# Kernel tuning notes

Measured on AMD Instinct MI355X. Metric: run time of the kernel, lower is better.

## Reference

```python
import jax, jax.numpy as jnp
import numpy as np

# HBV parameter bounds, in the order of self.parameters_bound
BOUNDS = np.array([
    [1.0, 6.0],     # parBETA
    [50.0, 1000.0], # parFC
    [0.05, 0.9],    # parK0
    [0.01, 0.5],    # parK1
    [0.001, 0.2],   # parK2
    [0.2, 1.0],     # parLP
    [0.0, 10.0],    # parPERC
    [0.0, 100.0],   # parUZL
    [-2.5, 2.5],    # parTT
    [0.5, 10.0],    # parCFMAX
    [0.0, 0.1],     # parCFR
    [0.0, 0.2],     # parCWH
    [0.3, 5.0],     # parBETAET
    [0.0, 1.0],     # parC (capillary)
    [0.0, 20.0],    # parTRbound (unused in core recurrence)
    [0.0, 2500.0],  # parAc (unused in core recurrence)
], dtype=np.float32)
NEARZERO = 1e-5
LENF = 15  # unit-hydrograph length
ROUT_A_MAX = 2.9
ROUT_B_MAX = 6.5


def uh_gamma(a, b, lenF):
    # a, b: [Ngrid]; returns normalized gamma UH weights [lenF, Ngrid]
    aa = jax.nn.relu(a) + 0.1
    theta = jax.nn.relu(b) + 0.5
    tt = jnp.arange(0.5, float(lenF), dtype=jnp.float32)[:, None]  # [lenF,1]
    w = jnp.exp(-jax.scipy.special.gammaln(aa)) / (theta ** aa) * tt ** (aa - 1.0) * jnp.exp(-tt / theta)
    return w / w.sum(0)


def hbv_forward(x_hydro_model, params_raw, conv_params_hydro):
    # x_hydro_model: [T, N, 3] (P, Temp, PET); params_raw: [T, N, 16, M]; conv: [N, 2]
    T, N, _ = x_hydro_model.shape
    M = params_raw.shape[-1]
    b = jnp.asarray(BOUNDS)
    p = b[:, 0].reshape(1, 1, -1, 1) + params_raw * (b[:, 1] - b[:, 0]).reshape(1, 1, -1, 1)
    (BETA, FC, K0, K1, K2, LP, PERC, UZL, TT, CFMAX, CFR, CWH, BETAET, C) = [p[:, :, i, :] for i in range(14)]
    Pm = x_hydro_model[:, :, 0:1]    # [T,N,1] broadcast vs nmul
    Tm = x_hydro_model[:, :, 1:2]
    PETm = x_hydro_model[:, :, 2:3]

    init = tuple(jnp.full((N, M), 0.001, jnp.float32) for _ in range(5))

    def step(carry, inp):
        SNOWPACK, MELTWATER, SM, SUZ, SLZ = carry
        (P_, Ta, PET_, BETA_, FC_, K0_, K1_, K2_, LP_, PERC_, UZL_, TT_, CFMAX_, CFR_, CWH_, BETAET_, C_) = inp
        RAIN = jnp.where(Ta >= TT_, P_, 0.0)
        SNOW = jnp.where(Ta < TT_, P_, 0.0)
        # snow routine
        SNOWPACK = SNOWPACK + SNOW
        melt = jnp.minimum(jnp.maximum(CFMAX_ * (Ta - TT_), 0.0), SNOWPACK)
        MELTWATER = MELTWATER + melt
        SNOWPACK = jnp.maximum(SNOWPACK - melt, NEARZERO)
        refreeze = jnp.minimum(jnp.maximum(CFR_ * CFMAX_ * (TT_ - Ta), 0.0), MELTWATER)
        SNOWPACK = SNOWPACK + refreeze
        MELTWATER = jnp.maximum(MELTWATER - refreeze, NEARZERO)
        tosoil = jnp.maximum(MELTWATER - CWH_ * SNOWPACK, 0.0)
        MELTWATER = jnp.maximum(MELTWATER - tosoil, NEARZERO)
        # soil routine
        soil_wet = jnp.clip((SM / FC_) ** BETA_, 0.0, 1.0)
        recharge = (RAIN + tosoil) * soil_wet
        SM = SM + RAIN + tosoil - recharge
        excess = jnp.maximum(SM - FC_, 0.0)
        SM = jnp.maximum(SM - excess, NEARZERO)
        evapfactor = jnp.clip((SM / (LP_ * FC_)) ** BETAET_, 0.0, 1.0)
        ETact = jnp.minimum(SM, PET_ * evapfactor)
        SM = jnp.maximum(SM - ETact, NEARZERO)
        # capillary rise from lower zone (parC)
        capillary = jnp.minimum(SLZ, C_ * SLZ * (1.0 - jnp.minimum(SM / FC_, 1.0)))
        SM = SM + capillary
        SLZ = jnp.maximum(SLZ - capillary, NEARZERO)
        # response routine
        SUZ = SUZ + recharge + excess
        PERCa = jnp.minimum(SUZ, PERC_)
        SUZ = SUZ - PERCa
        Q0 = K0_ * jnp.maximum(SUZ - UZL_, 0.0)
        SUZ = SUZ - Q0
        Q1 = K1_ * SUZ
        SUZ = SUZ - Q1
        SLZ = SLZ + PERCa
        Q2 = K2_ * SLZ
        SLZ = SLZ - Q2
        Qt = (Q0 + Q1 + Q2).mean(-1)  # average over nmul components -> [N]
        return (SNOWPACK, MELTWATER, SM, SUZ, SLZ), Qt

    _, Qsim = jax.lax.scan(step, init, (Pm, Tm, PETm, BETA, FC, K0, K1, K2, LP, PERC, UZL, TT, CFMAX, CFR, CWH, BETAET, C))
    # gamma-UH routing (causal per-grid convolution)
    rout_a = conv_params_hydro[:, 0] * ROUT_A_MAX
    rout_b = conv_params_hydro[:, 1] * ROUT_B_MAX
    UH = uh_gamma(rout_a, rout_b, LENF)  # [LENF, N]
    Qpad = jnp.pad(Qsim, ((LENF - 1, 0), (0, 0)))  # [T+LENF-1, N]
    Qrout = jnp.zeros_like(Qsim)
    for k in range(LENF):  # small fixed kernel length
        Qrout = Qrout + UH[k][None, :] * Qpad[LENF - 1 - k: LENF - 1 - k + T]
    return Qrout  # [T, N]


def setup_inputs() -> dict:
    key = jax.random.key(0)
    k1, k2, k3, k4, k5 = jax.random.split(key, 5)
    T, N, NP, M = 365, 4000, 16, 4
    P = jax.random.uniform(k1, (T, N), jnp.float32) * 15.0        # precip mm/day
    Temp = jax.random.uniform(k2, (T, N), jnp.float32) * 35.0 - 10.0  # deg C
    PET = jax.random.uniform(k3, (T, N), jnp.float32) * 6.0       # mm/day
    x_hydro_model = jnp.stack([P, Temp, PET], axis=-1)             # [T,N,3]
    params_raw = jax.random.uniform(k4, (T, N, NP, M), jnp.float32)
    conv_params_hydro = jax.random.uniform(k5, (N, 2), jnp.float32)
    return {"x_hydro_model": x_hydro_model, "params_raw": params_raw, "conv_params_hydro": conv_params_hydro}


def reference(x_hydro_model, params_raw, conv_params_hydro):
    return hbv_forward(x_hydro_model, params_raw, conv_params_hydro)
```

## Files before the change

### kernel.cpp

```cpp
#include <hip/hip_runtime.h>
#include <math.h>

#define NEARZERO 1e-5f
#define LENF 15

#define KB 7
#define CHUNK_STRIDE (1024 + 16)
#define SLOT_PARAM (4 * CHUNK_STRIDE)
#define SLOT_BYTES (SLOT_PARAM + 192)
#define BUF_BYTES (KB * SLOT_BYTES)
#define LDS_BYTES (2 * BUF_BYTES)

#define WAIT_VMCNT_35 0x8F73
#define WAIT_LGKM_0   0xC07F

#define GPTR(p) ((const __attribute__((address_space(1))) void*)(p))
#define LPTR(p) ((__attribute__((address_space(3))) void*)(p))

__device__ __forceinline__ float qswap1(float v) {
    return __int_as_float(__builtin_amdgcn_update_dpp(
        0, __float_as_int(v), 0xB1 , 0xF, 0xF, true));
}
__device__ __forceinline__ float qswap2(float v) {
    return __int_as_float(__builtin_amdgcn_update_dpp(
        0, __float_as_int(v), 0x4E , 0xF, 0xF, true));
}

__device__ __forceinline__ float powpos(float x, float y) {
    return __builtin_amdgcn_exp2f(y * __builtin_amdgcn_logf(x));
}

__device__ __forceinline__ void stage_batch(const float* __restrict__ praw,
                                            const float* __restrict__ x,
                                            char* smem, int buf, int t0,
                                            int T, int N, int n0, int lane)
{
    char* bufp = smem + buf * BUF_BYTES;
    for (int s = 0; s < KB; ++s) {
        int ts = t0 + s;
        if (ts > T - 1) ts = T - 1;
        const float* gp = praw + (size_t)ts * (size_t)(N * 64) + (size_t)n0 * 64;
        char* sp = bufp + s * SLOT_BYTES;
#pragma unroll
        for (int c = 0; c < 4; ++c) {
            __builtin_amdgcn_global_load_lds(GPTR(gp + c * 256 + lane * 4),
                                             LPTR(sp + c * CHUNK_STRIDE),
                                             16, 0, 0);
        }
        const float* xg = x + (size_t)ts * (size_t)(N * 3) + (size_t)n0 * 3;
        if (lane < 48) {
            __builtin_amdgcn_global_load_lds(GPTR(xg + lane),
                                             LPTR(sp + SLOT_PARAM),
                                             4, 0, 0);
        }
    }
}

__device__ __forceinline__ float dostep(const float* __restrict__ pr,
                                        float P, float Ta, float PET,
                                        float& SNOWPACK, float& MELTWATER,
                                        float& SM, float& SUZ, float& SLZ)
{
    const float BETA   = fmaf(pr[0],  5.0f,   1.0f);
    const float FC     = fmaf(pr[1],  950.0f, 50.0f);
    const float K0     = fmaf(pr[2],  0.85f,  0.05f);
    const float K1     = fmaf(pr[3],  0.49f,  0.01f);
    const float K2     = fmaf(pr[4],  0.199f, 0.001f);
    const float LP     = fmaf(pr[5],  0.8f,   0.2f);
    const float PERC   = pr[6] * 10.0f;
    const float UZL    = pr[7] * 100.0f;
    const float TT     = __fadd_rn(-2.5f, __fmul_rn(pr[8], 5.0f));
    const float CFMAX  = fmaf(pr[9],  9.5f,   0.5f);
    const float CFR    = pr[10] * 0.1f;
    const float CWH    = pr[11] * 0.2f;
    const float BETAET = fmaf(pr[12], 4.7f,   0.3f);
    const float C      = pr[13];

    const bool  wet  = (Ta >= TT);
    const float RAIN = wet ? P : 0.0f;
    const float SNOW = wet ? 0.0f : P;

    SNOWPACK += SNOW;
    const float melt = fminf(fmaxf(CFMAX * (Ta - TT), 0.0f), SNOWPACK);
    MELTWATER += melt;
    SNOWPACK = fmaxf(SNOWPACK - melt, NEARZERO);
    const float refreeze = fminf(fmaxf(CFR * CFMAX * (TT - Ta), 0.0f), MELTWATER);
    SNOWPACK += refreeze;
    MELTWATER = fmaxf(MELTWATER - refreeze, NEARZERO);
    const float tosoil = fmaxf(MELTWATER - CWH * SNOWPACK, 0.0f);
    MELTWATER = fmaxf(MELTWATER - tosoil, NEARZERO);

    const float rFC = __frcp_rn(FC);
    float soil_wet = powpos(SM * rFC, BETA);
    soil_wet = fminf(fmaxf(soil_wet, 0.0f), 1.0f);
    const float recharge = (RAIN + tosoil) * soil_wet;
    SM = SM + RAIN + tosoil - recharge;
    const float excess = fmaxf(SM - FC, 0.0f);
    SM = fmaxf(SM - excess, NEARZERO);

    float evapfactor = powpos(SM * __frcp_rn(LP * FC), BETAET);
    evapfactor = fminf(fmaxf(evapfactor, 0.0f), 1.0f);
    const float ETact = fminf(SM, PET * evapfactor);
    SM = fmaxf(SM - ETact, NEARZERO);

    const float capillary = fminf(SLZ, C * SLZ * (1.0f - fminf(SM * rFC, 1.0f)));
    SM += capillary;
    SLZ = fmaxf(SLZ - capillary, NEARZERO);

    SUZ = SUZ + recharge + excess;
    const float PERCa = fminf(SUZ, PERC);
    SUZ -= PERCa;
    const float Q0 = K0 * fmaxf(SUZ - UZL, 0.0f);
    SUZ -= Q0;
    const float Q1 = K1 * SUZ;
    SUZ -= Q1;
    SLZ += PERCa;
    const float Q2 = K2 * SLZ;
    SLZ -= Q2;
    return Q0 + Q1 + Q2;
}

__global__ void __launch_bounds__(64, 1)
hbv_kernel(const float* __restrict__ x,
           const float* __restrict__ praw,
           const float* __restrict__ conv,
           float* __restrict__ out,
           int T, int N)
{
    __shared__ __align__(16) char smem[LDS_BYTES];

    const int lane = threadIdx.x;
    const int n0 = blockIdx.x * 16;
    const int nl = lane >> 2;
    const int m  = lane & 3;
    const int n  = n0 + nl;
    const int pofs = (nl >> 2) * (CHUNK_STRIDE / 4) + (nl & 3) * 64 + m;
    const int xofs = (SLOT_PARAM / 4) + 3 * nl;

    const float a  = conv[2 * n + 0] * 2.9f;
    const float b  = conv[2 * n + 1] * 6.5f;
    const float aa = fmaxf(a, 0.0f) + 0.1f;
    const float th = fmaxf(b, 0.0f) + 0.5f;
    const float c0 = expf(-lgammaf(aa)) / powf(th, aa);
    float UH[LENF];
    float wsum = 0.0f;
#pragma unroll
    for (int k = 0; k < LENF; ++k) {
        const float tt = (float)k + 0.5f;
        const float w = c0 * powf(tt, aa - 1.0f) * expf(-tt / th);
        UH[k] = w;
        wsum += w;
    }
    const float rs = 1.0f / wsum;
#pragma unroll
    for (int k = 0; k < LENF; ++k) UH[k] *= rs;

    float acc[LENF - 1];
#pragma unroll
    for (int k = 0; k < LENF - 1; ++k) acc[k] = 0.0f;

    float SNOWPACK = 0.001f, MELTWATER = 0.001f, SM = 0.001f,
          SUZ = 0.001f, SLZ = 0.001f;

    stage_batch(praw, x, smem, 0, 0,  T, N, n0, lane);
    stage_batch(praw, x, smem, 1, KB, T, N, n0, lane);

    float pA[14], fA[3], pB[14], fB[3];

#define LOAD_SLOT(P, F, SIDX)                                                 \
    {                                                                         \
        const float* slotf = (const float*)(bufp + (SIDX) * SLOT_BYTES);      \
        const float* pp = slotf + pofs;                                       \
        _Pragma("unroll")                                                     \
        for (int i = 0; i < 14; ++i) P[i] = pp[4 * i];                        \
        const float* xs = slotf + xofs;                                       \
        F[0] = xs[0]; F[1] = xs[1]; F[2] = xs[2];                             \
    }

#define STEP(P, F, TIDX)                                                      \
    {                                                                         \
        float v = dostep(P, F[0], F[1], F[2],                                 \
                         SNOWPACK, MELTWATER, SM, SUZ, SLZ);                  \
        v += qswap1(v);                                                       \
        v += qswap2(v);                                                       \
        const float q = v * 0.25f;                                            \
        const float e = fmaf(UH[0], q, acc[0]);                               \
        _Pragma("unroll")                                                     \
        for (int k = 0; k < LENF - 2; ++k)                                    \
            acc[k] = fmaf(UH[k + 1], q, acc[k + 1]);                          \
        acc[LENF - 2] = UH[LENF - 1] * q;                                     \
        if (m == 0) out[(size_t)(TIDX) * N + n] = e;                          \
    }

    const int nb_full = T / KB;
    int t = 0;
    for (int bb = 0; bb < nb_full; ++bb) {
        __builtin_amdgcn_s_waitcnt(WAIT_VMCNT_35);
        __builtin_amdgcn_sched_barrier(0);

        const char* bufp = smem + (bb & 1) * BUF_BYTES;
        LOAD_SLOT(pA, fA, 0);
        LOAD_SLOT(pB, fB, 1);
        STEP(pA, fA, t + 0);
        LOAD_SLOT(pA, fA, 2);
        STEP(pB, fB, t + 1);
        LOAD_SLOT(pB, fB, 3);
        STEP(pA, fA, t + 2);
        LOAD_SLOT(pA, fA, 4);
        STEP(pB, fB, t + 3);
        LOAD_SLOT(pB, fB, 5);
        STEP(pA, fA, t + 4);
        LOAD_SLOT(pA, fA, 6);
        STEP(pB, fB, t + 5);
        STEP(pA, fA, t + 6);
        t += KB;

        __builtin_amdgcn_s_waitcnt(WAIT_LGKM_0);
        __builtin_amdgcn_sched_barrier(0);
        stage_batch(praw, x, smem, bb & 1, (bb + 2) * KB, T, N, n0, lane);
    }

    if (t < T) {
        __builtin_amdgcn_s_waitcnt(WAIT_VMCNT_35);
        __builtin_amdgcn_sched_barrier(0);
        const char* bufp = smem + (nb_full & 1) * BUF_BYTES;
        for (int s = 0; s < KB && t < T; ++s, ++t) {
            LOAD_SLOT(pA, fA, s);
            STEP(pA, fA, t);
        }
    }
#undef LOAD_SLOT
#undef STEP
}

extern "C" void kernel_launch(void* const* d_in, const int* in_sizes, int n_in,
                              void* d_out, int out_size, void* d_ws, size_t ws_size,
                              hipStream_t stream)
{
    const float* x    = (const float*)d_in[0];
    const float* praw = (const float*)d_in[1];
    const float* conv = (const float*)d_in[2];
    float* out = (float*)d_out;

    const int N = in_sizes[2] / 2;
    const int T = in_sizes[0] / (3 * N);

    const int grid = (N + 15) / 16;
    hipLaunchKernelGGL(hbv_kernel, dim3(grid), dim3(64), 0, stream,
                       x, praw, conv, out, T, N);
}
```

Baseline: 504.7 us.

## Process two basin groups per wave with swizzled LDS staging and shallower prefetch

Each 64-lane wave now handles 32 basins instead of 16, running two independent HBV recurrences per lane (A and B) so their dependency chains interleave and hide latency. The parameter staging loads 8 chunks per timestep through an XOR-permuted lane mapping to avoid LDS bank conflicts. Batch depth drops from 7 to 2 steps, with a software-pipelined register double buffer. Reciprocals and unit-hydrograph math use fast approximate intrinsics. The grid is halved, which lowers wave-level parallelism across the GPU, and the last block's start is clamped so it overlaps the previous block.

```diff
diff --git a/kernel.cpp b/kernel.cpp
--- a/kernel.cpp
+++ b/kernel.cpp
@@ -4,14 +4,16 @@
 #define NEARZERO 1e-5f
 #define LENF 15
 
-#define KB 7
+#define KB 2
+#define NCHUNK 8
 #define CHUNK_STRIDE (1024 + 16)
-#define SLOT_PARAM (4 * CHUNK_STRIDE)
-#define SLOT_BYTES (SLOT_PARAM + 192)
+#define SLOT_PARAM (NCHUNK * CHUNK_STRIDE)
+#define SLOT_BYTES (SLOT_PARAM + 384)
 #define BUF_BYTES (KB * SLOT_BYTES)
 #define LDS_BYTES (2 * BUF_BYTES)
 
-#define WAIT_VMCNT_35 0x8F73
+#define WAIT_VMCNT_18 0x4F72
+#define WAIT_VMCNT_20 0x4F74
 #define WAIT_LGKM_0   0xC07F
 
 #define GPTR(p) ((const __attribute__((address_space(1))) void*)(p))
@@ -29,29 +31,31 @@
 __device__ __forceinline__ float powpos(float x, float y) {
     return __builtin_amdgcn_exp2f(y * __builtin_amdgcn_logf(x));
 }
-
-__device__ __forceinline__ void stage_batch(const float* __restrict__ praw,
-                                            const float* __restrict__ x,
+__device__ __forceinline__ float rcpf(float x) { return __builtin_amdgcn_rcpf(x); }
+
+__device__ __forceinline__ void stage_batch(const char* __restrict__ praw_b,
+                                            const char* __restrict__ x_b,
                                             char* smem, int buf, int t0,
-                                            int T, int N, int n0, int lane)
+                                            int T, int N, int n0, int lane,
+                                            int perm16)
 {
     char* bufp = smem + buf * BUF_BYTES;
     for (int s = 0; s < KB; ++s) {
         int ts = t0 + s;
         if (ts > T - 1) ts = T - 1;
-        const float* gp = praw + (size_t)ts * (size_t)(N * 64) + (size_t)n0 * 64;
+        const char* gp = praw_b + (size_t)ts * ((size_t)N * 256) + (size_t)n0 * 256;
         char* sp = bufp + s * SLOT_BYTES;
 #pragma unroll
-        for (int c = 0; c < 4; ++c) {
-            __builtin_amdgcn_global_load_lds(GPTR(gp + c * 256 + lane * 4),
+        for (int c = 0; c < NCHUNK; ++c) {
+            __builtin_amdgcn_global_load_lds(GPTR(gp + c * 1024 + perm16),
                                              LPTR(sp + c * CHUNK_STRIDE),
                                              16, 0, 0);
         }
-        const float* xg = x + (size_t)ts * (size_t)(N * 3) + (size_t)n0 * 3;
-        if (lane < 48) {
-            __builtin_amdgcn_global_load_lds(GPTR(xg + lane),
+        const char* xg = x_b + (size_t)ts * ((size_t)N * 12) + (size_t)n0 * 12;
+        if (lane < 24) {
+            __builtin_amdgcn_global_load_lds(GPTR(xg + lane * 16),
                                              LPTR(sp + SLOT_PARAM),
-                                             4, 0, 0);
+                                             16, 0, 0);
         }
     }
 }
@@ -90,7 +94,7 @@
     const float tosoil = fmaxf(MELTWATER - CWH * SNOWPACK, 0.0f);
     MELTWATER = fmaxf(MELTWATER - tosoil, NEARZERO);
 
-    const float rFC = __frcp_rn(FC);
+    const float rFC = rcpf(FC);
     float soil_wet = powpos(SM * rFC, BETA);
     soil_wet = fminf(fmaxf(soil_wet, 0.0f), 1.0f);
     const float recharge = (RAIN + tosoil) * soil_wet;
@@ -98,7 +102,7 @@
     const float excess = fmaxf(SM - FC, 0.0f);
     SM = fmaxf(SM - excess, NEARZERO);
 
-    float evapfactor = powpos(SM * __frcp_rn(LP * FC), BETAET);
+    float evapfactor = powpos(SM * rcpf(LP * FC), BETAET);
     evapfactor = fminf(fmaxf(evapfactor, 0.0f), 1.0f);
     const float ETact = fminf(SM, PET * evapfactor);
     SM = fmaxf(SM - ETact, NEARZERO);
@@ -120,6 +124,29 @@
     return Q0 + Q1 + Q2;
 }
 
+__device__ __forceinline__ void make_uh(float craw0, float craw1, float* UH)
+{
+    const float a  = craw0 * 2.9f;
+    const float b  = craw1 * 6.5f;
+    const float aa = fmaxf(a, 0.0f) + 0.1f;
+    const float th = fmaxf(b, 0.0f) + 0.5f;
+    const float L2E = 1.4426950408889634f;
+    const float c   = -lgammaf(aa) * L2E - aa * __builtin_amdgcn_logf(th);
+    const float rthL = rcpf(th) * L2E;
+    float wsum = 0.0f;
+#pragma unroll
+    for (int k = 0; k < LENF; ++k) {
+        const float tt   = (float)k + 0.5f;
+        const float l2tt = __builtin_log2f((float)k + 0.5f);
+        const float l2w  = fmaf(aa - 1.0f, l2tt, c) - tt * rthL;
+        UH[k] = __builtin_amdgcn_exp2f(l2w);
+        wsum += UH[k];
+    }
+    const float rs = rcpf(wsum);
+#pragma unroll
+    for (int k = 0; k < LENF; ++k) UH[k] *= rs;
+}
+
 __global__ void __launch_bounds__(64, 1)
 hbv_kernel(const float* __restrict__ x,
            const float* __restrict__ praw,
@@ -130,107 +157,114 @@
     __shared__ __align__(16) char smem[LDS_BYTES];
 
     const int lane = threadIdx.x;
-    const int n0 = blockIdx.x * 16;
-    const int nl = lane >> 2;
-    const int m  = lane & 3;
-    const int n  = n0 + nl;
-    const int pofs = (nl >> 2) * (CHUNK_STRIDE / 4) + (nl & 3) * 64 + m;
-    const int xofs = (SLOT_PARAM / 4) + 3 * nl;
-
-    const float a  = conv[2 * n + 0] * 2.9f;
-    const float b  = conv[2 * n + 1] * 6.5f;
-    const float aa = fmaxf(a, 0.0f) + 0.1f;
-    const float th = fmaxf(b, 0.0f) + 0.5f;
-    const float c0 = expf(-lgammaf(aa)) / powf(th, aa);
-    float UH[LENF];
-    float wsum = 0.0f;
-#pragma unroll
-    for (int k = 0; k < LENF; ++k) {
-        const float tt = (float)k + 0.5f;
-        const float w = c0 * powf(tt, aa - 1.0f) * expf(-tt / th);
-        UH[k] = w;
-        wsum += w;
-    }
-    const float rs = 1.0f / wsum;
-#pragma unroll
-    for (int k = 0; k < LENF; ++k) UH[k] *= rs;
-
-    float acc[LENF - 1];
-#pragma unroll
-    for (int k = 0; k < LENF - 1; ++k) acc[k] = 0.0f;
-
-    float SNOWPACK = 0.001f, MELTWATER = 0.001f, SM = 0.001f,
-          SUZ = 0.001f, SLZ = 0.001f;
-
-    stage_batch(praw, x, smem, 0, 0,  T, N, n0, lane);
-    stage_batch(praw, x, smem, 1, KB, T, N, n0, lane);
-
-    float pA[14], fA[3], pB[14], fB[3];
-
-#define LOAD_SLOT(P, F, SIDX)                                                 \
+    int n0 = blockIdx.x * 32;
+    if (n0 > N - 32) n0 = N - 32;
+    const int nlA = lane >> 2;
+    const int m   = lane & 3;
+    const int nA  = n0 + nlA;
+    const int nB  = nA + 16;
+    const int perm16 = (lane ^ ((lane >> 3) & 6)) << 4;
+
+    const int qA  = nlA & 3;
+    const int q0A = qA & 1, q1A = (qA >> 1) & 1;
+    const int colA = (nlA >> 2) * CHUNK_STRIDE + qA * 256 + m * 4;
+    const int colB = ((nlA + 16) >> 2) * CHUNK_STRIDE + qA * 256 + m * 4;
+    char *pA[4], *pB[4], *pfA, *pfB;
+#pragma unroll
+    for (int j = 0; j < 4; ++j) {
+        const int d = 64 * (((j >> 1) & 1) ^ q1A) + 32 * ((j & 1) ^ q0A);
+        pA[j] = smem + colA + d;
+        pB[j] = smem + colB + d;
+    }
+    pfA = smem + SLOT_PARAM + 12 * nlA;
+    pfB = smem + SLOT_PARAM + 12 * (nlA + 16);
+
+    float UHA[LENF], UHB[LENF];
+    make_uh(conv[2 * nA], conv[2 * nA + 1], UHA);
+    make_uh(conv[2 * nB], conv[2 * nB + 1], UHB);
+
+    float accA[LENF - 1], accB[LENF - 1];
+#pragma unroll
+    for (int k = 0; k < LENF - 1; ++k) { accA[k] = 0.0f; accB[k] = 0.0f; }
+
+    float SA0 = 0.001f, SA1 = 0.001f, SA2 = 0.001f, SA3 = 0.001f, SA4 = 0.001f;
+    float SB0 = 0.001f, SB1 = 0.001f, SB2 = 0.001f, SB3 = 0.001f, SB4 = 0.001f;
+
+    const char* praw_b = (const char*)praw;
+    const char* x_b    = (const char*)x;
+
+    stage_batch(praw_b, x_b, smem, 0, 0,  T, N, n0, lane, perm16);
+    stage_batch(praw_b, x_b, smem, 1, KB, T, N, n0, lane, perm16);
+
+    float p1A[14], f1A[3], p1B[14], f1B[3];
+    float p2A[14], f2A[3], p2B[14], f2B[3];
+
+#define LOADSLOT(P_A, F_A, P_B, F_B, SOFS)                                    \
     {                                                                         \
-        const float* slotf = (const float*)(bufp + (SIDX) * SLOT_BYTES);      \
-        const float* pp = slotf + pofs;                                       \
         _Pragma("unroll")                                                     \
-        for (int i = 0; i < 14; ++i) P[i] = pp[4 * i];                        \
-        const float* xs = slotf + xofs;                                       \
-        F[0] = xs[0]; F[1] = xs[1]; F[2] = xs[2];                             \
-    }
-
-#define STEP(P, F, TIDX)                                                      \
+        for (int i = 0; i < 14; ++i) {                                        \
+            const int j = 2 * ((i >> 2) & 1) + ((i >> 1) & 1);                \
+            const int o = (SOFS) + 128 * (i >> 3) + 16 * (i & 1);             \
+            P_A[i] = *(const float*)(pA[j] + o);                              \
+            P_B[i] = *(const float*)(pB[j] + o);                              \
+        }                                                                     \
+        _Pragma("unroll")                                                     \
+        for (int k = 0; k < 3; ++k) {                                         \
+            F_A[k] = *(const float*)(pfA + (SOFS) + 4 * k);                   \
+            F_B[k] = *(const float*)(pfB + (SOFS) + 4 * k);                   \
+        }                                                                     \
+    }
+
+#define STEPT(P_A, F_A, P_B, F_B, TIDX)                                       \
     {                                                                         \
-        float v = dostep(P, F[0], F[1], F[2],                                 \
-                         SNOWPACK, MELTWATER, SM, SUZ, SLZ);                  \
-        v += qswap1(v);                                                       \
-        v += qswap2(v);                                                       \
-        const float q = v * 0.25f;                                            \
-        const float e = fmaf(UH[0], q, acc[0]);                               \
+        float vA = dostep(P_A, F_A[0], F_A[1], F_A[2], SA0, SA1, SA2, SA3, SA4); \
+        float vB = dostep(P_B, F_B[0], F_B[1], F_B[2], SB0, SB1, SB2, SB3, SB4); \
+        vA += qswap1(vA);  vB += qswap1(vB);                                  \
+        vA += qswap2(vA);  vB += qswap2(vB);                                  \
+        const float qqA = vA * 0.25f, qqB = vB * 0.25f;                       \
+        const float eA = fmaf(UHA[0], qqA, accA[0]);                          \
+        const float eB = fmaf(UHB[0], qqB, accB[0]);                          \
         _Pragma("unroll")                                                     \
-        for (int k = 0; k < LENF - 2; ++k)                                    \
-            acc[k] = fmaf(UH[k + 1], q, acc[k + 1]);                          \
-        acc[LENF - 2] = UH[LENF - 1] * q;                                     \
-        if (m == 0) out[(size_t)(TIDX) * N + n] = e;                          \
-    }
-
-    const int nb_full = T / KB;
+        for (int k = 0; k < LENF - 2; ++k) {                                  \
+            accA[k] = fmaf(UHA[k + 1], qqA, accA[k + 1]);                     \
+            accB[k] = fmaf(UHB[k + 1], qqB, accB[k + 1]);                     \
+        }                                                                     \
+        accA[LENF - 2] = UHA[LENF - 1] * qqA;                                 \
+        accB[LENF - 2] = UHB[LENF - 1] * qqB;                                 \
+        if (m == 0) {                                                         \
+            out[(size_t)(TIDX) * N + nA] = eA;                                \
+            out[(size_t)(TIDX) * N + nB] = eB;                                \
+        }                                                                     \
+    }
+
+    __builtin_amdgcn_s_waitcnt(WAIT_VMCNT_18);
+    __builtin_amdgcn_sched_barrier(0);
+    LOADSLOT(p1A, f1A, p1B, f1B, 0);
+
+    int dl = BUF_BYTES;
     int t = 0;
-    for (int bb = 0; bb < nb_full; ++bb) {
-        __builtin_amdgcn_s_waitcnt(WAIT_VMCNT_35);
-        __builtin_amdgcn_sched_barrier(0);
-
-        const char* bufp = smem + (bb & 1) * BUF_BYTES;
-        LOAD_SLOT(pA, fA, 0);
-        LOAD_SLOT(pB, fB, 1);
-        STEP(pA, fA, t + 0);
-        LOAD_SLOT(pA, fA, 2);
-        STEP(pB, fB, t + 1);
-        LOAD_SLOT(pB, fB, 3);
-        STEP(pA, fA, t + 2);
-        LOAD_SLOT(pA, fA, 4);
-        STEP(pB, fB, t + 3);
-        LOAD_SLOT(pB, fB, 5);
-        STEP(pA, fA, t + 4);
-        LOAD_SLOT(pA, fA, 6);
-        STEP(pB, fB, t + 5);
-        STEP(pA, fA, t + 6);
-        t += KB;
-
+    const int nb = T / KB;
+    for (int bb = 0; bb < nb; ++bb) {
+        LOADSLOT(p2A, f2A, p2B, f2B, SLOT_BYTES);
+        STEPT(p1A, f1A, p1B, f1B, t);
         __builtin_amdgcn_s_waitcnt(WAIT_LGKM_0);
         __builtin_amdgcn_sched_barrier(0);
-        stage_batch(praw, x, smem, bb & 1, (bb + 2) * KB, T, N, n0, lane);
+        stage_batch(praw_b, x_b, smem, bb & 1, (bb + 2) * KB, T, N, n0, lane, perm16);
+        __builtin_amdgcn_s_waitcnt(WAIT_VMCNT_20);
+        __builtin_amdgcn_sched_barrier(0);
+#pragma unroll
+        for (int j = 0; j < 4; ++j) { pA[j] += dl; pB[j] += dl; }
+        pfA += dl; pfB += dl; dl = -dl;
+        LOADSLOT(p1A, f1A, p1B, f1B, 0);
+        STEPT(p2A, f2A, p2B, f2B, t + 1);
+        t += KB;
     }
 
     if (t < T) {
-        __builtin_amdgcn_s_waitcnt(WAIT_VMCNT_35);
-        __builtin_amdgcn_sched_barrier(0);
-        const char* bufp = smem + (nb_full & 1) * BUF_BYTES;
-        for (int s = 0; s < KB && t < T; ++s, ++t) {
-            LOAD_SLOT(pA, fA, s);
-            STEP(pA, fA, t);
-        }
-    }
-#undef LOAD_SLOT
-#undef STEP
+        STEPT(p1A, f1A, p1B, f1B, t);
+    }
+#undef LOADSLOT
+#undef STEPT
 }
 
 extern "C" void kernel_launch(void* const* d_in, const int* in_sizes, int n_in,
@@ -245,7 +279,7 @@
     const int N = in_sizes[2] / 2;
     const int T = in_sizes[0] / (3 * N);
 
-    const int grid = (N + 15) / 16;
+    const int grid = (N + 31) / 32;
     hipLaunchKernelGGL(hbv_kernel, dim3(grid), dim3(64), 0, stream,
                        x, praw, conv, out, T, N);
 }
```

Result: slower. 687.9 us (+36.3%).
